# Kernel optimization log

Measured on AMD Instinct MI355X. Metric: run time of the kernel, lower is better.

## Reference

```python
import jax, jax.numpy as jnp
import numpy as np

EPS = 1e-5

def _conv1x1(x, w, b):
    # x: [B,C,H,W], w: [O,C], b: [O]  (1x1 conv == channel matmul)
    return jnp.einsum('bchw,oc->bohw', x, w) + b[None, :, None, None]

def _bn_relu(y, gamma, beta, mean, var):
    inv = gamma / jnp.sqrt(var + EPS)
    return jax.nn.relu(y * inv[None, :, None, None] + (beta - mean * inv)[None, :, None, None])

def setup_inputs() -> dict:
    key = jax.random.key(0)
    ks = jax.random.split(key, 8)
    B, C, H, W = 8, 2048, 48, 48
    mid = C // 4  # k = 4 -> mid_ch = 512
    s_in = (2.0 / C) ** 0.5   # kaiming-like scale for 1x1 convs from C channels
    s_mid = (2.0 / mid) ** 0.5
    return {
        'x': jax.random.normal(ks[0], (B, C, H, W), jnp.float32),
        'f_w': jax.random.normal(ks[1], (mid, C), jnp.float32) * s_in,
        'f_b': jnp.zeros((mid,), jnp.float32),
        'f_gamma': jnp.ones((mid,), jnp.float32),
        'f_beta': jnp.zeros((mid,), jnp.float32),
        'f_mean': jnp.zeros((mid,), jnp.float32),
        'f_var': jnp.ones((mid,), jnp.float32),
        'g_w': jax.random.normal(ks[2], (mid, C), jnp.float32) * s_in,
        'g_b': jnp.zeros((mid,), jnp.float32),
        'g_gamma': jnp.ones((mid,), jnp.float32),
        'g_beta': jnp.zeros((mid,), jnp.float32),
        'g_mean': jnp.zeros((mid,), jnp.float32),
        'g_var': jnp.ones((mid,), jnp.float32),
        'h_w': jax.random.normal(ks[3], (mid, C), jnp.float32) * s_in,
        'h_b': jnp.zeros((mid,), jnp.float32),
        'v_w': jax.random.normal(ks[4], (C, mid), jnp.float32) * s_mid,
        'v_b': jnp.zeros((C,), jnp.float32),
    }

def reference(x, f_w, f_b, f_gamma, f_beta, f_mean, f_var,
              g_w, g_b, g_gamma, g_beta, g_mean, g_var,
              h_w, h_b, v_w, v_b):
    B, C, H, W = x.shape
    mid = f_w.shape[0]
    N = H * W
    f_x = _bn_relu(_conv1x1(x, f_w, f_b), f_gamma, f_beta, f_mean, f_var).reshape(B, mid, N)
    g_x = _bn_relu(_conv1x1(x, g_w, g_b), g_gamma, g_beta, g_mean, g_var).reshape(B, mid, N)
    h_x = _conv1x1(x, h_w, h_b).reshape(B, mid, N)
    # z = f_x^T @ g_x : [B, N, N]
    scores = jnp.einsum('bcn,bcm->bnm', f_x, g_x) * (mid ** -0.5)
    attn = jax.nn.softmax(scores, axis=-1)
    # z = attn @ h_x^T : [B, N, mid] -> [B, mid, H, W]
    z = jnp.einsum('bnm,bcm->bcn', attn, h_x).reshape(B, mid, H, W)
    z = jnp.einsum('bchw,oc->bohw', z, v_w) + v_b[None, :, None, None]
    return (z + x, attn)
```

## Files before the change

### kernel.cpp

```cpp
#include <hip/hip_runtime.h>
#include <math.h>

typedef unsigned short u16;
typedef unsigned short u16x8 __attribute__((ext_vector_type(8)));
typedef __bf16 bf16x8 __attribute__((ext_vector_type(8)));
typedef float f32x4 __attribute__((ext_vector_type(4)));

typedef __attribute__((address_space(1))) const unsigned int gu32;
typedef __attribute__((address_space(3))) unsigned int su32;

#define B_ 8
#define C_ 2048
#define MID_ 512
#define N_ 2304

static __device__ __forceinline__ u16 f2bf(float f) {
  union { float f; unsigned u; } c; c.f = f;
  unsigned u = c.u;
  u += 0x7fffu + ((u >> 16) & 1u);
  return (u16)(u >> 16);
}

__global__ __launch_bounds__(256) void prep_wall_k(
    const float* __restrict__ fw, const float* __restrict__ gw,
    const float* __restrict__ hw, u16* __restrict__ wall) {
  int idx = blockIdx.x * 256 + threadIdx.x;
  if (idx >= 1536 * 2048) return;
  int r = idx >> 11;
  float v = (r < 512) ? fw[idx] : (r < 1024) ? gw[idx - (512 << 11)] : hw[idx - (1024 << 11)];
  wall[idx] = f2bf(v);
}

__global__ __launch_bounds__(256) void prep_vw_k(const float* __restrict__ vw, u16* __restrict__ o) {
  int idx = blockIdx.x * 256 + threadIdx.x;
  if (idx < 2048 * 512) o[idx] = f2bf(vw[idx]);
}

__global__ __launch_bounds__(256) void prep_sb_k(
    const float* fb, const float* fg, const float* fbe, const float* fm, const float* fv,
    const float* gb, const float* gg, const float* gbe, const float* gm, const float* gv,
    float* __restrict__ scale, float* __restrict__ bias) {
  int i = blockIdx.x * 256 + threadIdx.x;
  if (i >= 1024) return;
  if (i < 512) {
    float inv = fg[i] / sqrtf(fv[i] + 1e-5f);
    scale[i] = inv; bias[i] = fb[i] * inv + fbe[i] - fm[i] * inv;
  } else {
    int j = i - 512;
    float inv = gg[j] / sqrtf(gv[j] + 1e-5f);
    scale[i] = inv; bias[i] = gb[j] * inv + gbe[j] - gm[j] * inv;
  }
}

__global__ __launch_bounds__(256) void transpose_x_k(const float* __restrict__ x, u16* __restrict__ xT) {
  __shared__ float tile[32][33];
  int b = blockIdx.z;
  int n0 = blockIdx.x * 32, c0 = blockIdx.y * 32;
  int tx = threadIdx.x & 31, ty = threadIdx.x >> 5;
  const float* xb = x + (size_t)b * C_ * N_;
  u16* xTb = xT + (size_t)b * N_ * C_;
  #pragma unroll
  for (int i = 0; i < 4; ++i)
    tile[ty + i * 8][tx] = xb[(size_t)(c0 + ty + i * 8) * N_ + n0 + tx];
  __syncthreads();
  #pragma unroll
  for (int i = 0; i < 4; ++i)
    xTb[(size_t)(n0 + ty + i * 8) * C_ + c0 + tx] = f2bf(tile[tx][ty + i * 8]);
}

#define EP_FG 0
#define EP_HB 1
#define EP_SCORE 2
#define EP_BF16 3
#define EP_FINAL 4

template<int EPI>
__global__ __launch_bounds__(512, 2) void gemm3_kernel(
    const u16* __restrict__ Ag, int lda, long long sA,
    const u16* __restrict__ Bg, int ldb, long long sB,
    void* __restrict__ Cg, int ldc, long long sC, int K,
    const float* __restrict__ ep_scale, const float* __restrict__ ep_bias,
    const float* __restrict__ ep_x, long long sX, float fscale)
{
  extern __shared__ __align__(16) u16 smem[];
  u16* As = smem;
  u16* Bs = smem + 4 * 256 * 32;

  const int tid = threadIdx.x;
  const int lane = tid & 63;
  const int wv = tid >> 6;
  const int b = blockIdx.z;
  const int m0 = blockIdx.y * 256;
  const int n0 = blockIdx.x * 256;
  const int wm = (wv >> 2) * 128;
  const int wn = (wv & 3) * 64;
  const int lr = lane & 15, lg = lane >> 4;

  const u16* Ab = Ag + (size_t)b * sA;
  const u16* Bb = Bg + (size_t)b * sB;

  const int nk = K >> 5;

  const int srow = lane >> 2;
  const int sch  = lane & 3;

  const int cA = ((lg ^ (((wm + lr) >> 1) & 3)) * 8);
  const int cB = ((lg ^ (((wn + lr) >> 1) & 3)) * 8);

  f32x4 acc[8][4];
  #pragma unroll
  for (int i = 0; i < 8; ++i)
    #pragma unroll
    for (int j = 0; j < 4; ++j)
      acc[i][j] = f32x4{0.f, 0.f, 0.f, 0.f};

  auto STAGE = [&](int slot, int kt) {
    #pragma unroll
    for (int j = 0; j < 2; ++j) {
      const int rb = j * 128 + wv * 16;
      const int arow = rb + srow;
      {
        const int gch = sch ^ ((arow >> 1) & 3);
        const u16* ga = Ab + (size_t)(m0 + arow) * lda + kt * 32 + gch * 8;
        __builtin_amdgcn_global_load_lds((gu32*)ga, (su32*)(As + (slot * 256 + rb) * 32), 16, 0, 0);
      }
      {
        const int gch = sch ^ ((arow >> 1) & 3);
        const u16* gb = Bb + (size_t)(n0 + arow) * ldb + kt * 32 + gch * 8;
        __builtin_amdgcn_global_load_lds((gu32*)gb, (su32*)(Bs + (slot * 256 + rb) * 32), 16, 0, 0);
      }
    }
  };

  STAGE(0, 0); STAGE(1, 1); STAGE(2, 2);

  for (int kt = 0; kt < nk; ++kt) {
    const int slot = kt & 3;
    if (kt < nk - 2)        asm volatile("s_waitcnt vmcnt(8)" ::: "memory");
    else if (kt == nk - 2)  asm volatile("s_waitcnt vmcnt(4)" ::: "memory");
    else                    asm volatile("s_waitcnt vmcnt(0)" ::: "memory");
    __builtin_amdgcn_s_barrier();

    const u16* Asl = As + slot * (256 * 32);
    const u16* Bsl = Bs + slot * (256 * 32);
    bf16x8 af[8], bf[4];
    #pragma unroll
    for (int mf = 0; mf < 8; ++mf)
      af[mf] = *(const bf16x8*)(Asl + (wm + mf * 16 + lr) * 32 + cA);
    #pragma unroll
    for (int nf = 0; nf < 4; ++nf)
      bf[nf] = *(const bf16x8*)(Bsl + (wn + nf * 16 + lr) * 32 + cB);

    if (kt + 3 < nk) STAGE((kt + 3) & 3, kt + 3);

    __builtin_amdgcn_s_setprio(1);
    #pragma unroll
    for (int mf = 0; mf < 8; ++mf)
      #pragma unroll
      for (int nf = 0; nf < 4; ++nf)
        acc[mf][nf] = __builtin_amdgcn_mfma_f32_16x16x32_bf16(af[mf], bf[nf], acc[mf][nf], 0, 0, 0);
    __builtin_amdgcn_s_setprio(0);
    asm volatile("s_waitcnt lgkmcnt(0)" ::: "memory");
  }

  u16*   C16 = (u16*)Cg + (size_t)b * sC;
  float* C32 = (float*)Cg + (size_t)b * sC;
  const float* xb = (EPI == EP_FINAL) ? (ep_x + (size_t)b * sX) : nullptr;
  #pragma unroll
  for (int mf = 0; mf < 8; ++mf) {
    #pragma unroll
    for (int nf = 0; nf < 4; ++nf) {
      #pragma unroll
      for (int r = 0; r < 4; ++r) {
        int row = m0 + wm + mf * 16 + lg * 4 + r;
        int col = n0 + wn + nf * 16 + lr;
        float v = acc[mf][nf][r];
        if constexpr (EPI == EP_FG) {
          v = v * ep_scale[col] + ep_bias[col];
          v = fmaxf(v, 0.f);
          C16[(size_t)row * ldc + col] = f2bf(v);
        } else if constexpr (EPI == EP_HB) {
          C16[(size_t)row * ldc + col] = f2bf(v + ep_bias[row]);
        } else if constexpr (EPI == EP_SCORE) {
          C32[(size_t)row * ldc + col] = v * fscale;
        } else if constexpr (EPI == EP_BF16) {
          C16[(size_t)row * ldc + col] = f2bf(v);
        } else {
          v += ep_bias[row] + xb[(size_t)row * ldc + col];
          C32[(size_t)row * ldc + col] = v;
        }
      }
    }
  }
}

__global__ __launch_bounds__(256) void softmax_k(float* __restrict__ attn, u16* __restrict__ P) {
  float* r = attn + (size_t)blockIdx.x * N_;
  u16* pr = P + (size_t)blockIdx.x * N_;
  const int tid = threadIdx.x;
  float v[9];
  float mx = -3.0e38f;
  #pragma unroll
  for (int j = 0; j < 9; ++j) { v[j] = r[tid + j * 256]; mx = fmaxf(mx, v[j]); }
  #pragma unroll
  for (int o = 32; o; o >>= 1) mx = fmaxf(mx, __shfl_xor(mx, o));
  __shared__ float red[4], red2[4];
  if ((tid & 63) == 0) red[tid >> 6] = mx;
  __syncthreads();
  mx = fmaxf(fmaxf(red[0], red[1]), fmaxf(red[2], red[3]));
  float s = 0.f;
  #pragma unroll
  for (int j = 0; j < 9; ++j) { v[j] = __expf(v[j] - mx); s += v[j]; }
  #pragma unroll
  for (int o = 32; o; o >>= 1) s += __shfl_xor(s, o);
  if ((tid & 63) == 0) red2[tid >> 6] = s;
  __syncthreads();
  s = red2[0] + red2[1] + red2[2] + red2[3];
  float inv = 1.0f / s;
  #pragma unroll
  for (int j = 0; j < 9; ++j) {
    float o = v[j] * inv;
    r[tid + j * 256] = o;
    pr[tid + j * 256] = f2bf(o);
  }
}

extern "C" void kernel_launch(void* const* d_in, const int* in_sizes, int n_in,
                              void* d_out, int out_size, void* d_ws, size_t ws_size,
                              hipStream_t stream) {
  const float* x    = (const float*)d_in[0];
  const float* f_w  = (const float*)d_in[1];
  const float* f_b  = (const float*)d_in[2];
  const float* f_ga = (const float*)d_in[3];
  const float* f_be = (const float*)d_in[4];
  const float* f_me = (const float*)d_in[5];
  const float* f_va = (const float*)d_in[6];
  const float* g_w  = (const float*)d_in[7];
  const float* g_b  = (const float*)d_in[8];
  const float* g_ga = (const float*)d_in[9];
  const float* g_be = (const float*)d_in[10];
  const float* g_me = (const float*)d_in[11];
  const float* g_va = (const float*)d_in[12];
  const float* h_w  = (const float*)d_in[13];
  const float* h_b  = (const float*)d_in[14];
  const float* v_w  = (const float*)d_in[15];
  const float* v_b  = (const float*)d_in[16];

  float* out0 = (float*)d_out;
  float* attn = out0 + (size_t)B_ * C_ * N_;

  char* p = (char*)d_ws;
  u16* xT   = (u16*)p; p += (size_t)B_ * N_ * C_ * 2;
  u16* fghT = (u16*)p; p += (size_t)B_ * N_ * 1024 * 2;
  u16* hx   = (u16*)p; p += (size_t)B_ * MID_ * N_ * 2;
  u16* ZT   = (u16*)p; p += (size_t)B_ * N_ * MID_ * 2;
  u16* Wall = (u16*)p; p += (size_t)1536 * C_ * 2;
  u16* vwb  = (u16*)p; p += (size_t)C_ * MID_ * 2;
  float* sc = (float*)p; p += 1024 * 4;
  float* bi = (float*)p; p += 1024 * 4;
  u16* P = xT;

  hipFuncSetAttribute((const void*)gemm3_kernel<EP_FG>,    hipFuncAttributeMaxDynamicSharedMemorySize, 131072);
  hipFuncSetAttribute((const void*)gemm3_kernel<EP_HB>,    hipFuncAttributeMaxDynamicSharedMemorySize, 131072);
  hipFuncSetAttribute((const void*)gemm3_kernel<EP_SCORE>, hipFuncAttributeMaxDynamicSharedMemorySize, 131072);
  hipFuncSetAttribute((const void*)gemm3_kernel<EP_BF16>,  hipFuncAttributeMaxDynamicSharedMemorySize, 131072);
  hipFuncSetAttribute((const void*)gemm3_kernel<EP_FINAL>, hipFuncAttributeMaxDynamicSharedMemorySize, 131072);

  prep_wall_k<<<(1536 * 2048 + 255) / 256, 256, 0, stream>>>(f_w, g_w, h_w, Wall);
  prep_vw_k<<<(2048 * 512 + 255) / 256, 256, 0, stream>>>(v_w, vwb);
  prep_sb_k<<<4, 256, 0, stream>>>(f_b, f_ga, f_be, f_me, f_va,
                                   g_b, g_ga, g_be, g_me, g_va, sc, bi);
  transpose_x_k<<<dim3(N_ / 32, C_ / 32, B_), 256, 0, stream>>>(x, xT);

  gemm3_kernel<EP_FG><<<dim3(1024 / 256, N_ / 256, B_), 512, 131072, stream>>>(
      xT, C_, (long long)N_ * C_, Wall, C_, 0,
      fghT, 1024, (long long)N_ * 1024, C_, sc, bi, nullptr, 0, 0.f);

  gemm3_kernel<EP_HB><<<dim3(N_ / 256, MID_ / 256, B_), 512, 131072, stream>>>(
      Wall + (size_t)1024 * C_, C_, 0, xT, C_, (long long)N_ * C_,
      hx, N_, (long long)MID_ * N_, C_, nullptr, h_b, nullptr, 0, 0.f);

  const float fscale = 0.044194173824159216f;
  gemm3_kernel<EP_SCORE><<<dim3(N_ / 256, N_ / 256, B_), 512, 131072, stream>>>(
      fghT, 1024, (long long)N_ * 1024, fghT + 512, 1024, (long long)N_ * 1024,
      attn, N_, (long long)N_ * N_, MID_, nullptr, nullptr, nullptr, 0, fscale);

  softmax_k<<<B_ * N_, 256, 0, stream>>>(attn, P);

  gemm3_kernel<EP_BF16><<<dim3(MID_ / 256, N_ / 256, B_), 512, 131072, stream>>>(
      P, N_, (long long)N_ * N_, hx, N_, (long long)MID_ * N_,
      ZT, MID_, (long long)N_ * MID_, N_, nullptr, nullptr, nullptr, 0, 0.f);

  gemm3_kernel<EP_FINAL><<<dim3(N_ / 256, C_ / 256, B_), 512, 131072, stream>>>(
      vwb, MID_, 0, ZT, MID_, (long long)N_ * MID_,
      out0, N_, (long long)C_ * N_, MID_, nullptr, v_b, x, (long long)C_ * N_, 0.f);
}
```

Measured before the change: 562.3 us.

## Merge h projection into fused f/g GEMM and vectorize transpose and softmax

The h-projection GEMM is folded into the f/g projection GEMM by widening the output to 1536 columns. The h columns get a unit scale, their bias and no ReLU, and a small bf16 transpose kernel then rewrites them into the [mid,N] layout the attention GEMM expects. The x transpose now uses 64x64 tiles with float4 loads and 8-wide bf16 stores, and softmax uses float4/u16x4 vector memory accesses. This removes one GEMM launch and reduces global memory transactions, at the cost of an extra transpose pass over h and a wider fghT buffer.

```diff
diff --git a/kernel.cpp b/kernel.cpp
--- a/kernel.cpp
+++ b/kernel.cpp
@@ -2,6 +2,7 @@
 #include <math.h>
 
 typedef unsigned short u16;
+typedef unsigned short u16x4 __attribute__((ext_vector_type(4)));
 typedef unsigned short u16x8 __attribute__((ext_vector_type(8)));
 typedef __bf16 bf16x8 __attribute__((ext_vector_type(8)));
 typedef float f32x4 __attribute__((ext_vector_type(4)));
@@ -39,37 +40,61 @@
 __global__ __launch_bounds__(256) void prep_sb_k(
     const float* fb, const float* fg, const float* fbe, const float* fm, const float* fv,
     const float* gb, const float* gg, const float* gbe, const float* gm, const float* gv,
-    float* __restrict__ scale, float* __restrict__ bias) {
+    const float* hb, float* __restrict__ scale, float* __restrict__ bias) {
   int i = blockIdx.x * 256 + threadIdx.x;
-  if (i >= 1024) return;
+  if (i >= 1536) return;
   if (i < 512) {
     float inv = fg[i] / sqrtf(fv[i] + 1e-5f);
     scale[i] = inv; bias[i] = fb[i] * inv + fbe[i] - fm[i] * inv;
-  } else {
+  } else if (i < 1024) {
     int j = i - 512;
     float inv = gg[j] / sqrtf(gv[j] + 1e-5f);
     scale[i] = inv; bias[i] = gb[j] * inv + gbe[j] - gm[j] * inv;
+  } else {
+    scale[i] = 1.0f; bias[i] = hb[i - 1024];
   }
 }
 
 __global__ __launch_bounds__(256) void transpose_x_k(const float* __restrict__ x, u16* __restrict__ xT) {
-  __shared__ float tile[32][33];
-  int b = blockIdx.z;
-  int n0 = blockIdx.x * 32, c0 = blockIdx.y * 32;
-  int tx = threadIdx.x & 31, ty = threadIdx.x >> 5;
+  __shared__ float tile[64][68];
+  const int b = blockIdx.z;
+  const int n0 = blockIdx.x * 64, c0 = blockIdx.y * 64;
   const float* xb = x + (size_t)b * C_ * N_;
   u16* xTb = xT + (size_t)b * N_ * C_;
+  const int r = threadIdx.x >> 2, q = threadIdx.x & 3;
+  #pragma unroll
+  for (int j = 0; j < 4; ++j) {
+    float4 v = *(const float4*)&xb[(size_t)(c0 + r) * N_ + n0 + (q + 4 * j) * 4];
+    *(float4*)&tile[r][(q + 4 * j) * 4] = v;
+  }
+  __syncthreads();
+  #pragma unroll
+  for (int g = 0; g < 2; ++g) {
+    const int cl = (q * 2 + g) * 8;
+    u16x8 w;
+    #pragma unroll
+    for (int e = 0; e < 8; ++e) w[e] = f2bf(tile[cl + e][r]);
+    *(u16x8*)&xTb[(size_t)(n0 + r) * C_ + c0 + cl] = w;
+  }
+}
+
+__global__ __launch_bounds__(256) void transpose_h_k(const u16* __restrict__ fghT, u16* __restrict__ hx) {
+  __shared__ u16 tile[32][33];
+  const int b = blockIdx.z;
+  const int n0 = blockIdx.x * 32, c0 = blockIdx.y * 32;
+  const u16* src = fghT + (size_t)b * N_ * 1536;
+  u16* dst = hx + (size_t)b * MID_ * N_;
+  const int tx = threadIdx.x & 31, ty = threadIdx.x >> 5;
   #pragma unroll
   for (int i = 0; i < 4; ++i)
-    tile[ty + i * 8][tx] = xb[(size_t)(c0 + ty + i * 8) * N_ + n0 + tx];
+    tile[ty + i * 8][tx] = src[(size_t)(n0 + ty + i * 8) * 1536 + 1024 + c0 + tx];
   __syncthreads();
   #pragma unroll
   for (int i = 0; i < 4; ++i)
-    xTb[(size_t)(n0 + ty + i * 8) * C_ + c0 + tx] = f2bf(tile[tx][ty + i * 8]);
+    dst[(size_t)(c0 + ty + i * 8) * N_ + n0 + tx] = tile[tx][ty + i * 8];
 }
 
 #define EP_FG 0
-#define EP_HB 1
 #define EP_SCORE 2
 #define EP_BF16 3
 #define EP_FINAL 4
@@ -177,10 +202,8 @@
         float v = acc[mf][nf][r];
         if constexpr (EPI == EP_FG) {
           v = v * ep_scale[col] + ep_bias[col];
-          v = fmaxf(v, 0.f);
+          if (col < 1024) v = fmaxf(v, 0.f);
           C16[(size_t)row * ldc + col] = f2bf(v);
-        } else if constexpr (EPI == EP_HB) {
-          C16[(size_t)row * ldc + col] = f2bf(v + ep_bias[row]);
         } else if constexpr (EPI == EP_SCORE) {
           C32[(size_t)row * ldc + col] = v * fscale;
         } else if constexpr (EPI == EP_BF16) {
@@ -198,31 +221,40 @@
   float* r = attn + (size_t)blockIdx.x * N_;
   u16* pr = P + (size_t)blockIdx.x * N_;
   const int tid = threadIdx.x;
-  float v[9];
-  float mx = -3.0e38f;
-  #pragma unroll
-  for (int j = 0; j < 9; ++j) { v[j] = r[tid + j * 256]; mx = fmaxf(mx, v[j]); }
+  float4 v0 = *(const float4*)&r[tid * 4];
+  float4 v1 = *(const float4*)&r[1024 + tid * 4];
+  float  v2 = r[2048 + tid];
+  float mx = fmaxf(fmaxf(fmaxf(v0.x, v0.y), fmaxf(v0.z, v0.w)),
+                   fmaxf(fmaxf(fmaxf(v1.x, v1.y), fmaxf(v1.z, v1.w)), v2));
   #pragma unroll
   for (int o = 32; o; o >>= 1) mx = fmaxf(mx, __shfl_xor(mx, o));
   __shared__ float red[4], red2[4];
   if ((tid & 63) == 0) red[tid >> 6] = mx;
   __syncthreads();
   mx = fmaxf(fmaxf(red[0], red[1]), fmaxf(red[2], red[3]));
-  float s = 0.f;
-  #pragma unroll
-  for (int j = 0; j < 9; ++j) { v[j] = __expf(v[j] - mx); s += v[j]; }
+  v0.x = __expf(v0.x - mx); v0.y = __expf(v0.y - mx);
+  v0.z = __expf(v0.z - mx); v0.w = __expf(v0.w - mx);
+  v1.x = __expf(v1.x - mx); v1.y = __expf(v1.y - mx);
+  v1.z = __expf(v1.z - mx); v1.w = __expf(v1.w - mx);
+  v2 = __expf(v2 - mx);
+  float s = v0.x + v0.y + v0.z + v0.w + v1.x + v1.y + v1.z + v1.w + v2;
   #pragma unroll
   for (int o = 32; o; o >>= 1) s += __shfl_xor(s, o);
   if ((tid & 63) == 0) red2[tid >> 6] = s;
   __syncthreads();
   s = red2[0] + red2[1] + red2[2] + red2[3];
   float inv = 1.0f / s;
-  #pragma unroll
-  for (int j = 0; j < 9; ++j) {
-    float o = v[j] * inv;
-    r[tid + j * 256] = o;
-    pr[tid + j * 256] = f2bf(o);
-  }
+  v0.x *= inv; v0.y *= inv; v0.z *= inv; v0.w *= inv;
+  v1.x *= inv; v1.y *= inv; v1.z *= inv; v1.w *= inv;
+  v2 *= inv;
+  *(float4*)&r[tid * 4] = v0;
+  *(float4*)&r[1024 + tid * 4] = v1;
+  r[2048 + tid] = v2;
+  u16x4 p0; p0[0] = f2bf(v0.x); p0[1] = f2bf(v0.y); p0[2] = f2bf(v0.z); p0[3] = f2bf(v0.w);
+  u16x4 p1; p1[0] = f2bf(v1.x); p1[1] = f2bf(v1.y); p1[2] = f2bf(v1.z); p1[3] = f2bf(v1.w);
+  *(u16x4*)&pr[tid * 4] = p0;
+  *(u16x4*)&pr[1024 + tid * 4] = p1;
+  pr[2048 + tid] = f2bf(v2);
 }
 
 extern "C" void kernel_launch(void* const* d_in, const int* in_sizes, int n_in,
@@ -251,38 +283,35 @@
 
   char* p = (char*)d_ws;
   u16* xT   = (u16*)p; p += (size_t)B_ * N_ * C_ * 2;
-  u16* fghT = (u16*)p; p += (size_t)B_ * N_ * 1024 * 2;
+  u16* fghT = (u16*)p; p += (size_t)B_ * N_ * 1536 * 2;
   u16* hx   = (u16*)p; p += (size_t)B_ * MID_ * N_ * 2;
   u16* ZT   = (u16*)p; p += (size_t)B_ * N_ * MID_ * 2;
   u16* Wall = (u16*)p; p += (size_t)1536 * C_ * 2;
   u16* vwb  = (u16*)p; p += (size_t)C_ * MID_ * 2;
-  float* sc = (float*)p; p += 1024 * 4;
-  float* bi = (float*)p; p += 1024 * 4;
+  float* sc = (float*)p; p += 1536 * 4;
+  float* bi = (float*)p; p += 1536 * 4;
   u16* P = xT;
 
   hipFuncSetAttribute((const void*)gemm3_kernel<EP_FG>,    hipFuncAttributeMaxDynamicSharedMemorySize, 131072);
-  hipFuncSetAttribute((const void*)gemm3_kernel<EP_HB>,    hipFuncAttributeMaxDynamicSharedMemorySize, 131072);
   hipFuncSetAttribute((const void*)gemm3_kernel<EP_SCORE>, hipFuncAttributeMaxDynamicSharedMemorySize, 131072);
   hipFuncSetAttribute((const void*)gemm3_kernel<EP_BF16>,  hipFuncAttributeMaxDynamicSharedMemorySize, 131072);
   hipFuncSetAttribute((const void*)gemm3_kernel<EP_FINAL>, hipFuncAttributeMaxDynamicSharedMemorySize, 131072);
 
   prep_wall_k<<<(1536 * 2048 + 255) / 256, 256, 0, stream>>>(f_w, g_w, h_w, Wall);
   prep_vw_k<<<(2048 * 512 + 255) / 256, 256, 0, stream>>>(v_w, vwb);
-  prep_sb_k<<<4, 256, 0, stream>>>(f_b, f_ga, f_be, f_me, f_va,
-                                   g_b, g_ga, g_be, g_me, g_va, sc, bi);
-  transpose_x_k<<<dim3(N_ / 32, C_ / 32, B_), 256, 0, stream>>>(x, xT);
-
-  gemm3_kernel<EP_FG><<<dim3(1024 / 256, N_ / 256, B_), 512, 131072, stream>>>(
+  prep_sb_k<<<6, 256, 0, stream>>>(f_b, f_ga, f_be, f_me, f_va,
+                                   g_b, g_ga, g_be, g_me, g_va, h_b, sc, bi);
+  transpose_x_k<<<dim3(N_ / 64, C_ / 64, B_), 256, 0, stream>>>(x, xT);
+
+  gemm3_kernel<EP_FG><<<dim3(1536 / 256, N_ / 256, B_), 512, 131072, stream>>>(
       xT, C_, (long long)N_ * C_, Wall, C_, 0,
-      fghT, 1024, (long long)N_ * 1024, C_, sc, bi, nullptr, 0, 0.f);
-
-  gemm3_kernel<EP_HB><<<dim3(N_ / 256, MID_ / 256, B_), 512, 131072, stream>>>(
-      Wall + (size_t)1024 * C_, C_, 0, xT, C_, (long long)N_ * C_,
-      hx, N_, (long long)MID_ * N_, C_, nullptr, h_b, nullptr, 0, 0.f);
+      fghT, 1536, (long long)N_ * 1536, C_, sc, bi, nullptr, 0, 0.f);
+
+  transpose_h_k<<<dim3(N_ / 32, MID_ / 32, B_), 256, 0, stream>>>(fghT, hx);
 
   const float fscale = 0.044194173824159216f;
   gemm3_kernel<EP_SCORE><<<dim3(N_ / 256, N_ / 256, B_), 512, 131072, stream>>>(
-      fghT, 1024, (long long)N_ * 1024, fghT + 512, 1024, (long long)N_ * 1024,
+      fghT, 1536, (long long)N_ * 1536, fghT + 512, 1536, (long long)N_ * 1536,
       attn, N_, (long long)N_ * N_, MID_, nullptr, nullptr, nullptr, 0, fscale);
 
   softmax_k<<<B_ * N_, 256, 0, stream>>>(attn, P);
```

After: 518.8 us. -7.7%, faster.
